# Kernel tuning notes

Hardware: AMD Instinct MI355X
Metric: run time of the kernel (lower is better)

Reference implementation:

```python
import jax, jax.numpy as jnp
import numpy as np

B, N, D, H, DH = 4, 2048, 512, 8, 64  # batch, seqlen, hidden, heads, dim-per-head
EPS = 1e-5


def _layer_norm(x, g, b):
    m = jnp.mean(x, axis=-1, keepdims=True)
    v = jnp.var(x, axis=-1, keepdims=True)
    return (x - m) * jax.lax.rsqrt(v + EPS) * g + b


def setup_inputs() -> dict:
    key = jax.random.key(0)
    k0, k1, k2 = jax.random.split(key, 3)
    T = B * N
    return {
        "x": jax.random.normal(k0, (T, D), jnp.float32),
        "ln1_g": jnp.ones((D,), jnp.float32),
        "ln1_b": jnp.zeros((D,), jnp.float32),
        "w_uvqk": jax.random.normal(k1, (D, H * 4 * DH), jnp.float32) * 0.02,
        "ln2_g": jnp.ones((H * DH,), jnp.float32),
        "ln2_b": jnp.zeros((H * DH,), jnp.float32),
        "w_proj": jax.random.normal(k2, (H * DH, D), jnp.float32) * 0.02,
        "scaling_seqlen": N,
    }


def reference(x, ln1_g, ln1_b, w_uvqk, ln2_g, ln2_b, w_proj, scaling_seqlen):
    T = x.shape[0]
    # input layernorm -> fused uvqk projection -> SiLU
    normed_x = _layer_norm(x, ln1_g, ln1_b)
    silu_uvqk = jax.nn.silu(normed_x @ w_uvqk)          # [T, H*4*DH]
    silu_uvqk = silu_uvqk.reshape(T, H, 4 * DH)
    user, value, query, key = jnp.split(silu_uvqk, [DH, 2 * DH, 3 * DH], axis=-1)

    # jagged -> [B, N, H, DH] (equal-length sequences, offsets = i*N)
    q = query.reshape(B, N, H, DH)
    k = key.reshape(B, N, H, DH)
    v = value.reshape(B, N, H, DH)

    # HSTU attention: silu-gated (no softmax), causal, scaled by 1/scaling_seqlen
    scores = jnp.einsum('bnhd,bmhd->bhnm', q, k)        # [B, H, N, N]
    p = jax.nn.silu(scores) / jnp.float32(scaling_seqlen)
    causal = jnp.tril(jnp.ones((N, N), bool))
    p = jnp.where(causal, p, 0.0)
    attn = jnp.einsum('bhnm,bmhd->bnhd', p, v).reshape(T, H * DH)

    # output norm, user gate, projection, residual (dropout p=0.0 -> identity)
    normed_attn = _layer_norm(attn, ln2_g, ln2_b)
    user_flat = user.reshape(T, H * DH)
    out = (normed_attn * user_flat) @ w_proj + x
    return out
```

## Files before the change

kernel.cpp:

```cpp
#include <hip/hip_runtime.h>
#include <hip/hip_bf16.h>

typedef __bf16 bf16;
typedef __attribute__((ext_vector_type(8))) __bf16 bf16x8;
typedef __attribute__((ext_vector_type(4))) float f32x4;
typedef __attribute__((ext_vector_type(16))) float f32x16;

#define BB   4
#define NN   2048
#define DD   512
#define HH   8
#define DHH  64
#define TT   (BB*NN)
#define NUU  (HH*4*DHH)

#define AS1 __attribute__((address_space(1)))
#define AS3 __attribute__((address_space(3)))
__device__ __forceinline__ void gload16(const void* g, void* l){
  __builtin_amdgcn_global_load_lds((const AS1 void*)g, (AS3 void*)l, 16, 0, 0);
}

__device__ __forceinline__ float silu_fast(float x){
  return x * __builtin_amdgcn_rcpf(1.0f + __expf(-x));
}

__device__ __forceinline__ unsigned pk2(float a, float b){
  return (unsigned)__builtin_bit_cast(unsigned short, (bf16)a)
       | ((unsigned)__builtin_bit_cast(unsigned short, (bf16)b) << 16);
}

__device__ __forceinline__ void plswap(unsigned &a, unsigned &b){
  asm volatile("v_permlane32_swap_b32 %0, %1" : "+v"(a), "+v"(b));
}

__global__ void k_transpose_cast(const float* __restrict__ in, bf16* __restrict__ out,
                                 int R, int C){
  __shared__ float tile[32][33];
  int tx = threadIdx.x, ty = threadIdx.y;
  int c0 = blockIdx.x*32, r0 = blockIdx.y*32;
  #pragma unroll
  for (int i=0;i<4;i++) tile[ty+i*8][tx] = in[(size_t)(r0+ty+i*8)*C + c0+tx];
  __syncthreads();
  #pragma unroll
  for (int i=0;i<4;i++) out[(size_t)(c0+ty+i*8)*R + r0+tx] = (bf16)tile[tx][ty+i*8];
}

__global__ void k_ln_cast(const float* __restrict__ x, const float* __restrict__ g,
                          const float* __restrict__ bta, bf16* __restrict__ out){
  int lane = threadIdx.x & 63;
  int row  = blockIdx.x*4 + (threadIdx.x>>6);
  const float* xr = x + (size_t)row*512 + lane*8;
  float4 v0 = *(const float4*)xr;
  float4 v1 = *(const float4*)(xr+4);
  float vv[8] = {v0.x,v0.y,v0.z,v0.w,v1.x,v1.y,v1.z,v1.w};
  float s = 0.f, ss = 0.f;
  #pragma unroll
  for (int j=0;j<8;j++){ s += vv[j]; ss += vv[j]*vv[j]; }
  #pragma unroll
  for (int d=32; d; d>>=1){ s += __shfl_xor(s,d); ss += __shfl_xor(ss,d); }
  float m  = s * (1.f/512.f);
  float vr = ss * (1.f/512.f) - m*m;
  float rs = rsqrtf(vr + 1e-5f);
  const float* gp = g + lane*8;
  const float* bp = bta + lane*8;
  bf16x8 o;
  #pragma unroll
  for (int j=0;j<8;j++) o[j] = (bf16)((vv[j]-m)*rs*gp[j] + bp[j]);
  *(bf16x8*)(out + (size_t)row*512 + lane*8) = o;
}

__global__ void k_ln_gate(const float* __restrict__ attn, const float* __restrict__ g,
                          const float* __restrict__ bta, const bf16* __restrict__ uvqk,
                          bf16* __restrict__ out){
  int lane = threadIdx.x & 63;
  int row  = blockIdx.x*4 + (threadIdx.x>>6);
  const float* xr = attn + (size_t)row*512 + lane*8;
  float4 v0 = *(const float4*)xr;
  float4 v1 = *(const float4*)(xr+4);
  float vv[8] = {v0.x,v0.y,v0.z,v0.w,v1.x,v1.y,v1.z,v1.w};
  float s = 0.f, ss = 0.f;
  #pragma unroll
  for (int j=0;j<8;j++){ s += vv[j]; ss += vv[j]*vv[j]; }
  #pragma unroll
  for (int d=32; d; d>>=1){ s += __shfl_xor(s,d); ss += __shfl_xor(ss,d); }
  float m  = s * (1.f/512.f);
  float vr = ss * (1.f/512.f) - m*m;
  float rs = rsqrtf(vr + 1e-5f);
  const float* gp = g + lane*8;
  const float* bp = bta + lane*8;
  const bf16* up = uvqk + (size_t)row*NUU + (lane>>3)*256 + ((lane*8)&63);
  bf16x8 uu = *(const bf16x8*)up;
  bf16x8 o;
  #pragma unroll
  for (int j=0;j<8;j++)
    o[j] = (bf16)(((vv[j]-m)*rs*gp[j] + bp[j]) * (float)uu[j]);
  *(bf16x8*)(out + (size_t)row*512 + lane*8) = o;
}

template<int EPI>
__global__ __launch_bounds__(256) void k_gemm(const bf16* __restrict__ A,
                                              const bf16* __restrict__ BT,
                                              int Nd, const float* __restrict__ resid,
                                              void* __restrict__ Cout,
                                              bf16* __restrict__ vtout){
  __shared__ __align__(16) char smem[32768];
  char* As = smem;
  char* Bs = smem + 16384;
  const int K = 512;
  int t = threadIdx.x, lane = t & 63, wid = t >> 6;
  int wr = wid >> 1, wc = wid & 1;
  int lin = blockIdx.x;
  int wk  = (lin & 7)*((int)gridDim.x >> 3) + (lin >> 3);
  int nx  = Nd >> 7;
  int m0 = (wk / nx) * 128, n0 = (wk % nx) * 128;
  int blk = (lane & 7) ^ (lane >> 3);
  const bf16* gA = A  + (size_t)(m0 + wid*32 + (lane>>3))*K + blk*8;
  const bf16* gB = BT + (size_t)(n0 + wid*32 + (lane>>3))*K + blk*8;
  f32x4 acc[4][4] = {};
  for (int k0 = 0; k0 < K; k0 += 64){
    __syncthreads();
    #pragma unroll
    for (int c = 0; c < 4; ++c){
      gload16(gA + (size_t)c*8*K, As + wid*4096 + c*1024);
      gload16(gB + (size_t)c*8*K, Bs + wid*4096 + c*1024);
    }
    gA += 64; gB += 64;
    __syncthreads();
    #pragma unroll
    for (int kk = 0; kk < 64; kk += 32){
      int c0 = kk + (lane >> 4) * 8;
      bf16x8 a[4], b[4];
      #pragma unroll
      for (int i = 0; i < 4; i++){
        int ra = wr*64 + i*16 + (lane & 15);
        a[i] = *(const bf16x8*)(As + (((ra*64 + c0)*2) ^ ((ra & 7) << 4)));
        int rb = wc*64 + i*16 + (lane & 15);
        b[i] = *(const bf16x8*)(Bs + (((rb*64 + c0)*2) ^ ((rb & 7) << 4)));
      }
      #pragma unroll
      for (int i = 0; i < 4; i++)
        #pragma unroll
        for (int jj = 0; jj < 4; jj++)
          acc[i][jj] = __builtin_amdgcn_mfma_f32_16x16x32_bf16(a[i], b[jj], acc[i][jj], 0, 0, 0);
    }
  }
  bool isv = (EPI == 0) && ((n0 & 255) == 0) && (wc == 1);
  #pragma unroll
  for (int i = 0; i < 4; i++){
    #pragma unroll
    for (int jj = 0; jj < 4; jj++){
      int col = n0 + wc*64 + jj*16 + (lane & 15);
      if (EPI == 0){
        union { unsigned long long u; ushort s[4]; } pw;
        #pragma unroll
        for (int r = 0; r < 4; r++){
          int rowg = m0 + wr*64 + i*16 + (lane >> 4)*4 + r;
          float sv = silu_fast(acc[i][jj][r]);
          ((bf16*)Cout)[(size_t)rowg*Nd + col] = (bf16)sv;
          pw.s[r] = __builtin_bit_cast(ushort, (bf16)sv);
        }
        if (isv){
          int dh    = jj*16 + (lane & 15);
          int rowg0 = m0 + wr*64 + i*16 + (lane >> 4)*4;
          int bb = rowg0 >> 11, nn = rowg0 & (NN-1);
          int hh = n0 >> 8;
          *(unsigned long long*)(vtout + ((size_t)((bb*HH + hh)*64 + dh)*NN + nn)) = pw.u;
        }
      } else {
        #pragma unroll
        for (int r = 0; r < 4; r++){
          int rowg = m0 + wr*64 + i*16 + (lane >> 4)*4 + r;
          ((float*)Cout)[(size_t)rowg*Nd + col] = acc[i][jj][r] + resid[(size_t)rowg*Nd + col];
        }
      }
    }
  }
}

__global__ __launch_bounds__(256, 4) void k_attn(const bf16* __restrict__ uv,
                                                 const bf16* __restrict__ vt,
                                                 float* __restrict__ attn,
                                                 const int* __restrict__ scal){
  __shared__ __align__(16) char smem[32768];
  int t = threadIdx.x, lane = t & 63, w = t >> 6;
  int hi5 = lane >> 5;
  int lin  = blockIdx.x;
  int work = (lin & 7)*160 + (lin >> 3);
  int grp  = work / 40;
  int d    = 39 - (work % 40);
  int b = grp >> 3, h = grp & 7;
  int qt, ch;
  if (d < 4)       { qt = d;              ch = 0; }
  else if (d < 12) { qt = 4  + (d-4)/2;   ch = (d-4)&1; }
  else if (d < 24) { qt = 8  + (d-12)/3;  ch = (d-12)%3; }
  else             { qt = 12 + (d-24)/4;  ch = (d-24)&3; }
  int j0 = ch*8;
  int jmax = 2*qt + 1;
  int j1 = (jmax < j0+7) ? jmax : j0+7;
  int tok0 = b*NN + qt*128;
  float sinv = 1.0f / (float)(scal[0]);

  int blk  = (lane & 7) ^ (lane >> 3);
  int rsub = lane >> 3;

  {
    const bf16* gq = uv + (size_t)(tok0 + w*32 + rsub)*NUU + h*256 + 128 + blk*8;
    #pragma unroll
    for (int i = 0; i < 4; ++i)
      gload16(gq + (size_t)i*8*NUU, smem + 16384 + w*4096 + i*1024);
  }
  const bf16* gk = uv + (size_t)(b*NN + j0*64 + w*16 + rsub)*NUU + h*256 + 192 + blk*8;
  const bf16* gv = vt + (size_t)((b*HH + h)*64 + w*16 + rsub)*NN + j0*64 + blk*8;
  gload16(gk,                  smem + w*2048);
  gload16(gk + (size_t)8*NUU,  smem + w*2048 + 1024);
  gload16(gv,                  smem + 8192 + w*2048);
  gload16(gv + (size_t)8*NN,   smem + 8192 + w*2048 + 1024);
  gk += (size_t)64*NUU; gv += 64;
  asm volatile("s_waitcnt vmcnt(4)" ::: "memory");
  bf16x8 qfrag[4];
  {
    int rq = w*32 + (lane & 31);
    char* Qs = smem + 16384;
    #pragma unroll
    for (int ks = 0; ks < 4; ++ks){
      int c0 = ks*16 + hi5*8;
      qfrag[ks] = *(const bf16x8*)(Qs + (((rq*64 + c0)*2) ^ ((rq & 7) << 4)));
    }
  }
  __syncthreads();

  f32x16 oacc[2] = {};
  int qmin  = qt*128 + w*32;
  int qglob = qmin + (lane & 31);
  int cur = 0;
  for (int j = j0; j <= j1; ++j){
    if (j < j1){
      gload16(gk,                 smem + (cur^1)*16384 + w*2048);
      gload16(gk + (size_t)8*NUU, smem + (cur^1)*16384 + w*2048 + 1024);
      gload16(gv,                 smem + (cur^1)*16384 + 8192 + w*2048);
      gload16(gv + (size_t)8*NN,  smem + (cur^1)*16384 + 8192 + w*2048 + 1024);
      gk += (size_t)64*NUU; gv += 64;
      asm volatile("s_waitcnt vmcnt(4)" ::: "memory");
    } else {
      asm volatile("s_waitcnt vmcnt(0)" ::: "memory");
    }
    __builtin_amdgcn_s_barrier();
    char* Ks = smem + cur*16384;
    char* Vs = Ks + 8192;
    #pragma unroll
    for (int sub = 0; sub < 2; ++sub){
      int kvbase = j*64 + sub*32;
      if (kvbase < qmin + 32){
        f32x16 sacc = {};
        int rk = sub*32 + (lane & 31);
        #pragma unroll
        for (int ks = 0; ks < 4; ++ks){
          int c0 = ks*16 + hi5*8;
          bf16x8 ak = *(const bf16x8*)(Ks + (((rk*64 + c0)*2) ^ ((rk & 7) << 4)));
          sacc = __builtin_amdgcn_mfma_f32_32x32x16_bf16(ak, qfrag[ks], sacc, 0, 0, 0);
        }
        union { unsigned u[8]; bf16x8 v[2]; } P;
        if (kvbase + 31 <= qmin){
          #pragma unroll
          for (int m = 0; m < 4; ++m){
            P.u[2*m]   = pk2(silu_fast(sacc[4*m+0]), silu_fast(sacc[4*m+1]));
            P.u[2*m+1] = pk2(silu_fast(sacc[4*m+2]), silu_fast(sacc[4*m+3]));
          }
        } else {
          #pragma unroll
          for (int m = 0; m < 4; ++m){
            float pr[4];
            #pragma unroll
            for (int r = 0; r < 4; ++r){
              int kvg = kvbase + 8*m + 4*hi5 + r;
              pr[r] = (kvg <= qglob) ? silu_fast(sacc[4*m+r]) : 0.0f;
            }
            P.u[2*m]   = pk2(pr[0], pr[1]);
            P.u[2*m+1] = pk2(pr[2], pr[3]);
          }
        }
        plswap(P.u[0], P.u[2]); plswap(P.u[1], P.u[3]);
        plswap(P.u[4], P.u[6]); plswap(P.u[5], P.u[7]);
        #pragma unroll
        for (int kh = 0; kh < 2; ++kh){
          int c0 = sub*32 + kh*16 + hi5*8;
          #pragma unroll
          for (int dsb = 0; dsb < 2; ++dsb){
            int rv = dsb*32 + (lane & 31);
            bf16x8 vb = *(const bf16x8*)(Vs + (((rv*64 + c0)*2) ^ ((rv & 7) << 4)));
            oacc[dsb] = __builtin_amdgcn_mfma_f32_32x32x16_bf16(P.v[kh], vb, oacc[dsb], 0, 0, 0);
          }
        }
      }
    }
    asm volatile("" ::: "memory");
    __builtin_amdgcn_s_barrier();
    cur ^= 1;
  }
  #pragma unroll
  for (int dsb = 0; dsb < 2; ++dsb){
    #pragma unroll
    for (int r = 0; r < 16; ++r){
      int qrow = (r & 3) + 4*hi5 + 8*(r >> 2);
      atomicAdd(&attn[(size_t)(tok0 + w*32 + qrow)*DD + h*64 + dsb*32 + (lane & 31)],
                oacc[dsb][r] * sinv);
    }
  }
}

extern "C" void kernel_launch(void* const* d_in, const int* in_sizes, int n_in,
                              void* d_out, int out_size, void* d_ws, size_t ws_size,
                              hipStream_t stream){
  (void)in_sizes; (void)n_in; (void)out_size; (void)ws_size;
  const float* x      = (const float*)d_in[0];
  const float* ln1_g  = (const float*)d_in[1];
  const float* ln1_b  = (const float*)d_in[2];
  const float* w_uvqk = (const float*)d_in[3];
  const float* ln2_g  = (const float*)d_in[4];
  const float* ln2_b  = (const float*)d_in[5];
  const float* w_proj = (const float*)d_in[6];
  const int*   scal   = (const int*)d_in[7];
  float* out = (float*)d_out;

  char* ws = (char*)d_ws;
  bf16*  wT1  = (bf16*)(ws);
  bf16*  wT2  = (bf16*)(ws + (2u<<20));
  bf16*  xn   = (bf16*)(ws + (2u<<20) + (512u<<10));
  bf16*  uvq  = (bf16*)(ws + (10u<<20) + (512u<<10));
  float* attn = (float*)(ws + (42u<<20) + (512u<<10));
  bf16*  vtb  = (bf16*)(ws + (58u<<20) + (512u<<10));

  hipMemsetAsync(attn, 0, (size_t)TT*DD*sizeof(float), stream);
  k_transpose_cast<<<dim3(64,16), dim3(32,8), 0, stream>>>(w_uvqk, wT1, 512, 2048);
  k_transpose_cast<<<dim3(16,16), dim3(32,8), 0, stream>>>(w_proj, wT2, 512, 512);
  k_ln_cast<<<TT/4, 256, 0, stream>>>(x, ln1_g, ln1_b, xn);
  k_gemm<0><<<dim3(1024), dim3(256), 0, stream>>>(xn, wT1, 2048, nullptr, (void*)uvq, vtb);
  k_attn<<<dim3(1280), dim3(256), 0, stream>>>(uvq, vtb, attn, scal);
  k_ln_gate<<<TT/4, 256, 0, stream>>>(attn, ln2_g, ln2_b, uvq, xn);
  k_gemm<1><<<dim3(256), dim3(256), 0, stream>>>(xn, wT2, 512, x, (void*)out, nullptr);
}
```

Before: 113.2 us.

## Use 256-row query tiles with 8-wave attention blocks and merge weight transposes

The attention kernel now processes 256 query rows per block with 512 threads (8 waves), so each K/V tile staged in LDS is shared by twice as many query rows. Work is rebalanced into 20 chunks per (batch, head) with even kv-range splits. Q fragments are loaded straight from global memory rather than through LDS, and the pipeline changes to a single barrier per iteration with wait-all before the prefetch. The two weight transpose launches are merged into one kernel to save a launch. The trade-off is fewer blocks and occupancy, and a possibly shallower overlap of loads with compute.

```diff
diff --git a/kernel.cpp b/kernel.cpp
--- a/kernel.cpp
+++ b/kernel.cpp
@@ -33,11 +33,15 @@
   asm volatile("v_permlane32_swap_b32 %0, %1" : "+v"(a), "+v"(b));
 }
 
-__global__ void k_transpose_cast(const float* __restrict__ in, bf16* __restrict__ out,
-                                 int R, int C){
+__global__ void k_transpose2(const float* __restrict__ w1, bf16* __restrict__ o1,
+                             const float* __restrict__ w2, bf16* __restrict__ o2){
   __shared__ float tile[32][33];
   int tx = threadIdx.x, ty = threadIdx.y;
-  int c0 = blockIdx.x*32, r0 = blockIdx.y*32;
+  int bx = blockIdx.x;
+  const float* in; bf16* out; int R, C, c0;
+  if (bx < 64){ in = w1; out = o1; R = 512; C = 2048; c0 = bx*32; }
+  else        { in = w2; out = o2; R = 512; C = 512;  c0 = (bx-64)*32; }
+  int r0 = blockIdx.y*32;
   #pragma unroll
   for (int i=0;i<4;i++) tile[ty+i*8][tx] = in[(size_t)(r0+ty+i*8)*C + c0+tx];
   __syncthreads();
@@ -177,76 +181,62 @@
   }
 }
 
-__global__ __launch_bounds__(256, 4) void k_attn(const bf16* __restrict__ uv,
-                                                 const bf16* __restrict__ vt,
-                                                 float* __restrict__ attn,
-                                                 const int* __restrict__ scal){
+__global__ __launch_bounds__(512) void k_attn(const bf16* __restrict__ uv,
+                                              const bf16* __restrict__ vt,
+                                              float* __restrict__ attn,
+                                              const int* __restrict__ scal){
   __shared__ __align__(16) char smem[32768];
   int t = threadIdx.x, lane = t & 63, w = t >> 6;
   int hi5 = lane >> 5;
   int lin  = blockIdx.x;
-  int work = (lin & 7)*160 + (lin >> 3);
-  int grp  = work / 40;
-  int d    = 39 - (work % 40);
+  int work = (lin & 7)*80 + (lin >> 3);
+  int grp  = work / 20;
+  int d    = 19 - (work % 20);
   int b = grp >> 3, h = grp & 7;
   int qt, ch;
-  if (d < 4)       { qt = d;              ch = 0; }
-  else if (d < 12) { qt = 4  + (d-4)/2;   ch = (d-4)&1; }
-  else if (d < 24) { qt = 8  + (d-12)/3;  ch = (d-12)%3; }
-  else             { qt = 12 + (d-24)/4;  ch = (d-24)&3; }
-  int j0 = ch*8;
-  int jmax = 2*qt + 1;
-  int j1 = (jmax < j0+7) ? jmax : j0+7;
-  int tok0 = b*NN + qt*128;
+  if (d < 2)       { qt = d;               ch = 0; }
+  else if (d < 6)  { qt = 2 + ((d-2)>>1);  ch = (d-2)&1; }
+  else if (d < 12) { qt = 4 + (d-6)/3;     ch = (d-6)%3; }
+  else             { qt = 6 + ((d-12)>>2); ch = (d-12)&3; }
+  int total = 4*qt + 4;
+  int nch   = (qt>>1) + 1;
+  int bsz   = total / nch, rem = total - bsz*nch;
+  int j0 = ch*bsz + (ch < rem ? ch : rem);
+  int j1 = j0 + bsz + (ch < rem ? 1 : 0) - 1;
+  int tok0 = b*NN + qt*256;
   float sinv = 1.0f / (float)(scal[0]);
 
   int blk  = (lane & 7) ^ (lane >> 3);
   int rsub = lane >> 3;
 
-  {
-    const bf16* gq = uv + (size_t)(tok0 + w*32 + rsub)*NUU + h*256 + 128 + blk*8;
-    #pragma unroll
-    for (int i = 0; i < 4; ++i)
-      gload16(gq + (size_t)i*8*NUU, smem + 16384 + w*4096 + i*1024);
-  }
-  const bf16* gk = uv + (size_t)(b*NN + j0*64 + w*16 + rsub)*NUU + h*256 + 192 + blk*8;
-  const bf16* gv = vt + (size_t)((b*HH + h)*64 + w*16 + rsub)*NN + j0*64 + blk*8;
-  gload16(gk,                  smem + w*2048);
-  gload16(gk + (size_t)8*NUU,  smem + w*2048 + 1024);
-  gload16(gv,                  smem + 8192 + w*2048);
-  gload16(gv + (size_t)8*NN,   smem + 8192 + w*2048 + 1024);
-  gk += (size_t)64*NUU; gv += 64;
-  asm volatile("s_waitcnt vmcnt(4)" ::: "memory");
   bf16x8 qfrag[4];
   {
-    int rq = w*32 + (lane & 31);
-    char* Qs = smem + 16384;
-    #pragma unroll
-    for (int ks = 0; ks < 4; ++ks){
-      int c0 = ks*16 + hi5*8;
-      qfrag[ks] = *(const bf16x8*)(Qs + (((rq*64 + c0)*2) ^ ((rq & 7) << 4)));
-    }
-  }
-  __syncthreads();
+    const bf16* gq = uv + (size_t)(tok0 + w*32 + (lane & 31))*NUU + h*256 + 128 + hi5*8;
+    #pragma unroll
+    for (int ks = 0; ks < 4; ++ks)
+      qfrag[ks] = *(const bf16x8*)(gq + ks*16);
+  }
+  const bf16* gk = uv + (size_t)(b*NN + j0*64 + w*8 + rsub)*NUU + h*256 + 192 + blk*8;
+  const bf16* gv = vt + (size_t)((b*HH + h)*64 + w*8 + rsub)*NN + j0*64 + blk*8;
+  gload16(gk, smem + w*1024);
+  gload16(gv, smem + 8192 + w*1024);
+  gk += (size_t)64*NUU; gv += 64;
 
   f32x16 oacc[2] = {};
-  int qmin  = qt*128 + w*32;
+  int qmin  = qt*256 + w*32;
   int qglob = qmin + (lane & 31);
   int cur = 0;
   for (int j = j0; j <= j1; ++j){
+    asm volatile("s_waitcnt vmcnt(0)" ::: "memory");
+    __builtin_amdgcn_s_barrier();
     if (j < j1){
-      gload16(gk,                 smem + (cur^1)*16384 + w*2048);
-      gload16(gk + (size_t)8*NUU, smem + (cur^1)*16384 + w*2048 + 1024);
-      gload16(gv,                 smem + (cur^1)*16384 + 8192 + w*2048);
-      gload16(gv + (size_t)8*NN,  smem + (cur^1)*16384 + 8192 + w*2048 + 1024);
+      char* nb = smem + (cur^1)*16384;
+      gload16(gk, nb + w*1024);
+      gload16(gv, nb + 8192 + w*1024);
       gk += (size_t)64*NUU; gv += 64;
-      asm volatile("s_waitcnt vmcnt(4)" ::: "memory");
-    } else {
-      asm volatile("s_waitcnt vmcnt(0)" ::: "memory");
-    }
-    __builtin_amdgcn_s_barrier();
-    char* Ks = smem + cur*16384;
-    char* Vs = Ks + 8192;
+    }
+    const char* Ks = smem + cur*16384;
+    const char* Vs = Ks + 8192;
     #pragma unroll
     for (int sub = 0; sub < 2; ++sub){
       int kvbase = j*64 + sub*32;
@@ -293,8 +283,6 @@
         }
       }
     }
-    asm volatile("" ::: "memory");
-    __builtin_amdgcn_s_barrier();
     cur ^= 1;
   }
   #pragma unroll
@@ -331,11 +319,10 @@
   bf16*  vtb  = (bf16*)(ws + (58u<<20) + (512u<<10));
 
   hipMemsetAsync(attn, 0, (size_t)TT*DD*sizeof(float), stream);
-  k_transpose_cast<<<dim3(64,16), dim3(32,8), 0, stream>>>(w_uvqk, wT1, 512, 2048);
-  k_transpose_cast<<<dim3(16,16), dim3(32,8), 0, stream>>>(w_proj, wT2, 512, 512);
+  k_transpose2<<<dim3(80,16), dim3(32,8), 0, stream>>>(w_uvqk, wT1, w_proj, wT2);
   k_ln_cast<<<TT/4, 256, 0, stream>>>(x, ln1_g, ln1_b, xn);
   k_gemm<0><<<dim3(1024), dim3(256), 0, stream>>>(xn, wT1, 2048, nullptr, (void*)uvq, vtb);
-  k_attn<<<dim3(1280), dim3(256), 0, stream>>>(uvq, vtb, attn, scal);
+  k_attn<<<dim3(640), dim3(512), 0, stream>>>(uvq, vtb, attn, scal);
   k_ln_gate<<<TT/4, 256, 0, stream>>>(attn, ln2_g, ln2_b, uvq, xn);
   k_gemm<1><<<dim3(256), dim3(256), 0, stream>>>(xn, wT2, 512, x, (void*)out, nullptr);
 }
```

New measurement: 116.5 us. 1.03x slower.
